# Kernel optimization log

Measured on AMD Instinct MI355X. Metric: run time of the kernel, lower is better.

## Reference

```python
import jax, jax.numpy as jnp
import numpy as np

B, N, C = 4, 1024, 1024
H, TD, MULT = 16, 256, 4
HD = C // H
MAX_LEN = 1024
EPS = 1e-5


def _layer_norm(x, g, b):
    m = jnp.mean(x, axis=-1, keepdims=True)
    v = jnp.mean((x - m) ** 2, axis=-1, keepdims=True)
    return (x - m) / jnp.sqrt(v + EPS) * g + b


def _skew(x):
    # x: [B,H,N,M] -> pad left on last dim, reshape, drop first row -> [B,H,N,M]
    b, h, n, m = x.shape
    x = jnp.pad(x, ((0, 0), (0, 0), (0, 0), (1, 0)))
    x = x.reshape(b, h, m + 1, n)
    return x[:, :, 1:, :]


def setup_inputs() -> dict:
    key = jax.random.key(0)
    ks = jax.random.split(key, 16)
    s = 0.02
    return {
        "x": jax.random.normal(ks[0], (B, N, C), jnp.float32),
        "t": jax.random.normal(ks[1], (B, TD), jnp.float32),
        "ln1_g": jnp.ones((C,), jnp.float32),
        "ln1_b": jnp.zeros((C,), jnp.float32),
        "qkv_w": jax.random.normal(ks[2], (C, 3 * C), jnp.float32) * s,
        "qkv_b": jnp.zeros((3 * C,), jnp.float32),
        "time_w": jax.random.normal(ks[3], (TD, 3 * C), jnp.float32) * s,
        "time_b": jnp.zeros((3 * C,), jnp.float32),
        "out_w": jax.random.normal(ks[4], (C, C), jnp.float32) * s,
        "out_b": jnp.zeros((C,), jnp.float32),
        "Er": jax.random.normal(ks[5], (MAX_LEN, HD), jnp.float32) * s,
        "ln2_g": jnp.ones((C,), jnp.float32),
        "ln2_b": jnp.zeros((C,), jnp.float32),
        "ff1_w": jax.random.normal(ks[6], (C, MULT * C), jnp.float32) * s,
        "ff1_b": jnp.zeros((MULT * C,), jnp.float32),
        "ff2_w": jax.random.normal(ks[7], (MULT * C, C), jnp.float32) * s,
        "ff2_b": jnp.zeros((C,), jnp.float32),
    }


def reference(x, t, ln1_g, ln1_b, qkv_w, qkv_b, time_w, time_b, out_w, out_b,
              Er, ln2_g, ln2_b, ff1_w, ff1_b, ff2_w, ff2_b):
    # ---- attention branch ----
    xn = _layer_norm(x, ln1_g, ln1_b)
    qkv = (xn @ qkv_w + qkv_b).reshape(B, N, 3, H, HD).transpose(2, 0, 3, 1, 4)
    q, k, v = qkv[0], qkv[1], qkv[2]  # [B,H,N,HD]
    tqkv = (t @ time_w + time_b).reshape(B, 1, 3, H, HD).transpose(2, 0, 3, 1, 4)
    q = q + tqkv[0]
    k = k + tqkv[1]
    v = v + tqkv[2]
    Er_n = Er[MAX_LEN - N:]  # [N,HD]
    rel = jnp.einsum('bhnd,md->bhnm', q, Er_n)
    rel = _skew(rel)
    scale = HD ** -0.5
    attn = jnp.einsum('bhnd,bhmd->bhnm', q, k) * scale + rel
    attn = jax.nn.softmax(attn, axis=-1)
    out = jnp.einsum('bhnm,bhmd->bhnd', attn, v)
    out = out.transpose(0, 2, 1, 3).reshape(B, N, C)
    x = x + (out @ out_w + out_b)
    # ---- FFN branch ----
    h = _layer_norm(x, ln2_g, ln2_b)
    h = jax.nn.gelu(h @ ff1_w + ff1_b, approximate=False)
    x = x + (h @ ff2_w + ff2_b)
    return x
```

## Files before the change

### kernel.cpp

```cpp
#include <hip/hip_runtime.h>
#include <hip/hip_bf16.h>

typedef __attribute__((ext_vector_type(8))) short short8;
typedef __attribute__((ext_vector_type(4))) float f32x4;
typedef __attribute__((ext_vector_type(16))) float f32x16;

#define DEV __device__ __forceinline__

DEV float bf2f(ushort u){ union { float f; unsigned int i; } x; x.i = ((unsigned int)u)<<16; return x.f; }
DEV ushort f2bf(float f){ union { float fl; unsigned int i; } x; x.fl = f; unsigned int r = x.i + 0x7fffu + ((x.i>>16)&1u); return (ushort)(r>>16); }

DEV void gl2lds16(const ushort* g, ushort* l){
  __builtin_amdgcn_global_load_lds((const __attribute__((address_space(1))) void*)g,
                                   (__attribute__((address_space(3))) void*)l, 16, 0, 0);
}
DEV f32x16 mfma32(short8 a, short8 b, f32x16 c){
  return __builtin_amdgcn_mfma_f32_32x32x16_bf16(a, b, c, 0, 0, 0);
}
DEV uint cvtpk(float lo, float hi){
  uint r; asm("v_cvt_pk_bf16_f32 %0, %1, %2" : "=v"(r) : "v"(lo), "v"(hi));
  return r;
}
DEV uint q8(float v){
  float c = fminf(fmaxf(v, -127.f), 127.f);
  return ((uint)(int)rintf(c)) & 255u;
}

__global__ void cvt_f2b(const float* __restrict__ in, ushort* __restrict__ out, int n){
  int i = blockIdx.x*blockDim.x + threadIdx.x;
  int stride = gridDim.x*blockDim.x;
  for (; i < n; i += stride) out[i] = f2bf(in[i]);
}

__global__ __launch_bounds__(256) void wt_cvt(const float* __restrict__ in, ushort* __restrict__ out,
                                              int K, int N, int ldk){
  const int n0 = blockIdx.x*64, k0 = blockIdx.y*64;
  __shared__ float T[64][65];
  const int tid = threadIdx.x;
  const int r = tid>>4, c = (tid&15)*4;
  #pragma unroll
  for (int p=0;p<4;p++){
    float4 v = *(const float4*)&in[(size_t)(k0 + p*16 + r)*N + n0 + c];
    T[p*16+r][c+0]=v.x; T[p*16+r][c+1]=v.y; T[p*16+r][c+2]=v.z; T[p*16+r][c+3]=v.w;
  }
  __syncthreads();
  #pragma unroll
  for (int p=0;p<4;p++){
    int n = p*16 + r;
    ushort u0 = f2bf(T[c+0][n]), u1 = f2bf(T[c+1][n]), u2 = f2bf(T[c+2][n]), u3 = f2bf(T[c+3][n]);
    ushort4 u = make_ushort4(u0,u1,u2,u3);
    *(ushort4*)&out[(size_t)(n0+n)*ldk + k0 + c] = u;
  }
}

__global__ __launch_bounds__(256) void vt_k(const ushort* __restrict__ qkv, ushort* __restrict__ vt){
  const int bh = blockIdx.y; const int b = bh>>4, h = bh&15;
  const int n0 = blockIdx.x*64;
  __shared__ ushort T[64][66];
  const int tid = threadIdx.x;
  const int r = tid>>3, c8 = (tid&7)*8;
  #pragma unroll
  for (int p=0;p<2;p++){
    int row = p*32 + r;
    short8 v = *(const short8*)&qkv[(size_t)(b*1024 + n0 + row)*3200 + 2048 + h*64 + c8];
    #pragma unroll
    for (int i=0;i<8;i++) T[row][c8+i] = ((ushort*)&v)[i];
  }
  __syncthreads();
  #pragma unroll
  for (int p=0;p<2;p++){
    int d = p*32 + r;
    union { ushort u[8]; short8 v; } o;
    #pragma unroll
    for (int i=0;i<8;i++) o.u[i] = T[c8+i][d];
    *(short8*)&vt[(size_t)(bh*64 + d)*1152 + n0 + c8] = o.v;
  }
}

__global__ __launch_bounds__(256) void ln_rows(const float* __restrict__ in,
                                               const float* __restrict__ g,
                                               const float* __restrict__ bta,
                                               ushort* __restrict__ out, int ldo){
  int row = blockIdx.x; int tid = threadIdx.x;
  const float* x = in + (size_t)row*1024;
  float v[4]; float s = 0.f;
  #pragma unroll
  for (int i=0;i<4;i++){ v[i] = x[tid + 256*i]; s += v[i]; }
  __shared__ float rbuf[256];
  rbuf[tid] = s; __syncthreads();
  for (int off=128; off>0; off>>=1){ if (tid<off) rbuf[tid]+=rbuf[tid+off]; __syncthreads(); }
  float mean = rbuf[0] * (1.f/1024.f);
  __syncthreads();
  float s2 = 0.f;
  #pragma unroll
  for (int i=0;i<4;i++){ float d=v[i]-mean; s2 += d*d; }
  rbuf[tid] = s2; __syncthreads();
  for (int off=128; off>0; off>>=1){ if (tid<off) rbuf[tid]+=rbuf[tid+off]; __syncthreads(); }
  float var = rbuf[0] * (1.f/1024.f);
  float rstd = rsqrtf(var + 1e-5f);
  #pragma unroll
  for (int i=0;i<4;i++){ int c = tid+256*i; out[(size_t)row*ldo+c] = f2bf((v[i]-mean)*rstd*g[c]+bta[c]); }
}

__global__ __launch_bounds__(256) void tq_gemm2(const float* __restrict__ t, const float* __restrict__ tw,
                                                const float* __restrict__ tb, float* __restrict__ tq){
  const int tid = threadIdx.x;
  const int j = blockIdx.x*64 + (tid & 63);
  const int sl = tid >> 6;
  float acc[4] = {0.f,0.f,0.f,0.f};
  for (int k = sl*64; k < sl*64+64; ++k){
    float wv = tw[(size_t)k*3072 + j];
    #pragma unroll
    for (int b=0;b<4;b++) acc[b] = fmaf(t[b*256+k], wv, acc[b]);
  }
  __shared__ float red[4][4][64];
  #pragma unroll
  for (int b=0;b<4;b++) red[sl][b][tid&63] = acc[b];
  __syncthreads();
  if (sl == 0){
    #pragma unroll
    for (int b=0;b<4;b++)
      tq[b*3072 + j] = red[0][b][tid&63] + red[1][b][tid&63] + red[2][b][tid&63] + red[3][b][tid&63] + tb[j];
  }
}

template<int EPI, int TN>
__global__ __launch_bounds__(256) void gemm4(
    const ushort* __restrict__ A, const ushort* __restrict__ Bt,
    const float* __restrict__ bias, const float* __restrict__ extra,
    ushort* __restrict__ outb, float* __restrict__ outf,
    int K, int lda, int ldb, int ldo, int lde, int nbx)
{
  constexpr int NJ = TN/32;
  __shared__ __align__(16) ushort Al[2][128*32];
  __shared__ __align__(16) ushort Bl[2][TN*32];
  const int nwg = gridDim.x, cpx = nwg >> 3;
  const int bid = blockIdx.x;
  const int swz = (bid & 7)*cpx + (bid >> 3);
  const int m0 = (swz / nbx)*128, n0 = (swz % nbx)*TN;
  const int tid = threadIdx.x, lane = tid & 63, wid = tid >> 6;
  const int wm = (wid&1)*64, wn = (wid>>1)*(TN/2);
  const int l15 = lane&15, l4 = lane>>4;
  f32x4 acc[4][NJ];
  #pragma unroll
  for (int i=0;i<4;i++)
    #pragma unroll
    for (int jx=0;jx<NJ;jx++){ acc[i][jx][0]=0.f; acc[i][jx][1]=0.f; acc[i][jx][2]=0.f; acc[i][jx][3]=0.f; }
  const ushort* a0p = A + (size_t)(m0 + (tid>>2))*lda + (tid&3)*8;
  const ushort* a1p = A + (size_t)(m0 + 64 + (tid>>2))*lda + (tid&3)*8;
  const ushort* b0p = Bt + (size_t)(n0 + (tid>>2))*ldb + (tid&3)*8;
  const ushort* b1p = nullptr;
  if constexpr (TN==128) b1p = Bt + (size_t)(n0 + 64 + (tid>>2))*ldb + (tid&3)*8;
  const int lsl = tid*8, lsh = (tid+256)*8;

  gl2lds16(a0p, &Al[0][lsl]);
  gl2lds16(a1p, &Al[0][lsh]);
  gl2lds16(b0p, &Bl[0][lsl]);
  if constexpr (TN==128) gl2lds16(b1p, &Bl[0][lsh]);
  __syncthreads();

  const int nk = K >> 5;
  for (int it=0; it<nk; ++it){
    const int cur = it & 1;
    ushort* Ac = Al[cur];  ushort* Bc = Bl[cur];
    if (it+1 < nk){
      const int k1 = (it+1) << 5;
      gl2lds16(a0p + k1, &Al[cur^1][lsl]);
      gl2lds16(a1p + k1, &Al[cur^1][lsh]);
      gl2lds16(b0p + k1, &Bl[cur^1][lsl]);
      if constexpr (TN==128) gl2lds16(b1p + k1, &Bl[cur^1][lsh]);
    }
    short8 af[4], bfr[NJ];
    #pragma unroll
    for (int mi=0;mi<4;mi++) af[mi]  = *(const short8*)&Ac[(wm + mi*16 + l15)*32 + l4*8];
    #pragma unroll
    for (int nj=0;nj<NJ;nj++) bfr[nj] = *(const short8*)&Bc[(wn + nj*16 + l15)*32 + l4*8];
    #pragma unroll
    for (int mi=0;mi<4;mi++)
      #pragma unroll
      for (int nj=0;nj<NJ;nj++)
        acc[mi][nj] = __builtin_amdgcn_mfma_f32_16x16x32_bf16(af[mi], bfr[nj], acc[mi][nj], 0,0,0);
    __syncthreads();
  }
  #pragma unroll
  for (int mi=0;mi<4;mi++)
    #pragma unroll
    for (int nj=0;nj<NJ;nj++)
      #pragma unroll
      for (int j=0;j<4;j++){
        int row = m0 + wm + mi*16 + l4*4 + j;
        int col = n0 + wn + nj*16 + l15;
        float v = acc[mi][nj][j] + bias[col];
        if constexpr (EPI==0){ v += extra[(size_t)(row>>10)*lde + col]; outb[(size_t)row*ldo+col] = f2bf(v); }
        else if constexpr (EPI==1){ v += extra[(size_t)row*lde + col]; outf[(size_t)row*ldo+col] = v; }
        else { v = 0.5f*v*(1.f+erff(v*0.70710678118f)); outb[(size_t)row*ldo+col] = f2bf(v); }
      }
}

__global__ __launch_bounds__(256) void attn8b(
    const ushort* __restrict__ qkv, const ushort* __restrict__ Er,
    const ushort* __restrict__ Vt, ushort* __restrict__ out)
{
  const int bid0 = blockIdx.x;
  const int swz = (bid0 & 7)*256 + (bid0 >> 3);
  const int bh = swz >> 5, b = bh >> 4, h = bh & 15;
  const int rt = swz & 31;
  const int r0 = rt*32;
  const int tid = threadIdx.x, w = tid >> 6, lane = tid & 63;
  const int l31 = lane & 31, hi = lane >> 5;

  __shared__ __align__(16) signed char RRF8[34704];
  ushort* Obuf = (ushort*)RRF8;
  float*  ml   = (float*)(RRF8 + 34192);

  const ushort* Qp = qkv + (size_t)b*1024*3200 + h*64;
  const ushort* Kp = Qp + 1024;
  const ushort* Vp = Vt + (size_t)bh*64*1152;

  const int r = r0 + l31;
  short8 qf0 = *(const short8*)(Qp + (size_t)r*3200 +      hi*8);
  short8 qf1 = *(const short8*)(Qp + (size_t)r*3200 + 16 + hi*8);
  short8 qf2 = *(const short8*)(Qp + (size_t)r*3200 + 32 + hi*8);
  short8 qf3 = *(const short8*)(Qp + (size_t)r*3200 + 48 + hi*8);

  if (tid < 32) RRF8[tid*1036 + 1035] = 0;

  const float ESC = 92.332481f;
  for (int t=0; t<8; ++t){
    const int e0 = w*256 + t*32;
    const ushort* ep = Er + (size_t)(e0 + l31)*64 + hi*8;
    short8 ea0 = *(const short8*)(ep);
    short8 ea1 = *(const short8*)(ep + 16);
    short8 ea2 = *(const short8*)(ep + 32);
    short8 ea3 = *(const short8*)(ep + 48);
    f32x16 acc = {};
    acc = mfma32(ea0, qf0, acc);
    acc = mfma32(ea1, qf1, acc);
    acc = mfma32(ea2, qf2, acc);
    acc = mfma32(ea3, qf3, acc);
    #pragma unroll
    for (int q=0;q<4;q++){
      int e = e0 + 8*q + 4*hi;
      uint u = q8(acc[4*q+0]*ESC) | (q8(acc[4*q+1]*ESC)<<8)
             | (q8(acc[4*q+2]*ESC)<<16) | (q8(acc[4*q+3]*ESC)<<24);
      *(uint*)(RRF8 + l31*1036 + e) = u;
    }
  }
  {
    const int q32r = min(r0 + 32, 1023);
    const ushort* q32 = Qp + (size_t)q32r*3200;
    const int e4 = tid*4;
    float a[4] = {0.f,0.f,0.f,0.f};
    #pragma unroll
    for (int c8=0;c8<8;c8++){
      short8 qv = *(const short8*)(q32 + c8*8);
      float qx[8];
      #pragma unroll
      for (int i=0;i<8;i++) qx[i] = bf2f(((ushort*)&qv)[i]);
      #pragma unroll
      for (int e=0;e<4;e++){
        short8 ev = *(const short8*)(Er + (size_t)(e4+e)*64 + c8*8);
        #pragma unroll
        for (int i=0;i<8;i++) a[e] = fmaf(qx[i], bf2f(((ushort*)&ev)[i]), a[e]);
      }
    }
    uint u = q8(a[0]*ESC) | (q8(a[1]*ESC)<<8) | (q8(a[2]*ESC)<<16) | (q8(a[3]*ESC)<<24);
    *(uint*)(RRF8 + 33152 + e4) = u;
  }
  __syncthreads();

  const int rbase = l31*1036;
  const int kvbase = w*256;
  f32x16 O0 = {}, O1 = {};
  float lsum = 0.f;

  short8 kA0 = *(const short8*)(Kp + (size_t)(kvbase + l31)*3200 +      hi*8);
  short8 kA1 = *(const short8*)(Kp + (size_t)(kvbase + l31)*3200 + 16 + hi*8);
  short8 kA2 = *(const short8*)(Kp + (size_t)(kvbase + l31)*3200 + 32 + hi*8);
  short8 kA3 = *(const short8*)(Kp + (size_t)(kvbase + l31)*3200 + 48 + hi*8);
  short8 kB0, kB1, kB2, kB3;

  auto step = [&](short8& ka0, short8& ka1, short8& ka2, short8& ka3,
                  short8& kn0, short8& kn1, short8& kn2, short8& kn3, int t){
    const int c0 = kvbase + t*32;
    if (t < 7){
      const ushort* kp = Kp + (size_t)(c0 + 32 + l31)*3200 + hi*8;
      kn0 = *(const short8*)(kp);
      kn1 = *(const short8*)(kp + 16);
      kn2 = *(const short8*)(kp + 32);
      kn3 = *(const short8*)(kp + 48);
    }
    signed char bs[16];
    #pragma unroll
    for (int q=0;q<4;q++)
      #pragma unroll
      for (int j=0;j<4;j++){
        int c = c0 + 8*q + 4*hi + j;
        int d = c - r;
        int off = (d<=0) ? (1023+d) : (1034+d);
        bs[4*q+j] = RRF8[rbase + off];
      }
    short8 v00 = *(const short8*)(Vp + (size_t)l31*1152      + c0 +      hi*8);
    short8 v01 = *(const short8*)(Vp + (size_t)l31*1152      + c0 + 16 + hi*8);
    short8 v10 = *(const short8*)(Vp + (size_t)(32+l31)*1152 + c0 +      hi*8);
    short8 v11 = *(const short8*)(Vp + (size_t)(32+l31)*1152 + c0 + 16 + hi*8);
    f32x16 S = {};
    __builtin_amdgcn_s_setprio(1);
    S = mfma32(ka0, qf0, S);
    S = mfma32(ka1, qf1, S);
    S = mfma32(ka2, qf2, S);
    S = mfma32(ka3, qf3, S);
    __builtin_amdgcn_s_setprio(0);
    float p[16];
    float s0=0.f, s1=0.f, s2=0.f, s3=0.f;
    #pragma unroll
    for (int i=0;i<16;i++){
      p[i] = __builtin_amdgcn_exp2f(fmaf(S[i], 0.18033688f, (float)bs[i]*0.015625f));
      if ((i&3)==0) s0 += p[i]; else if ((i&3)==1) s1 += p[i];
      else if ((i&3)==2) s2 += p[i]; else s3 += p[i];
    }
    lsum += (s0+s1)+(s2+s3);
    uint W00=cvtpk(p[0],p[1]),   W01=cvtpk(p[2],p[3]);
    uint W10=cvtpk(p[4],p[5]),   W11=cvtpk(p[6],p[7]);
    uint W20=cvtpk(p[8],p[9]),   W21=cvtpk(p[10],p[11]);
    uint W30=cvtpk(p[12],p[13]), W31=cvtpk(p[14],p[15]);
    uint x00 = (uint)__shfl_xor((int)(hi? W00 : W10), 32, 64);
    uint x01 = (uint)__shfl_xor((int)(hi? W01 : W11), 32, 64);
    uint x10 = (uint)__shfl_xor((int)(hi? W20 : W30), 32, 64);
    uint x11 = (uint)__shfl_xor((int)(hi? W21 : W31), 32, 64);
    union { uint u[4]; short8 v; } pf0, pf1;
    pf0.u[0] = hi ? x00 : W00;  pf0.u[1] = hi ? x01 : W01;
    pf0.u[2] = hi ? W10 : x00;  pf0.u[3] = hi ? W11 : x01;
    pf1.u[0] = hi ? x10 : W20;  pf1.u[1] = hi ? x11 : W21;
    pf1.u[2] = hi ? W30 : x10;  pf1.u[3] = hi ? W31 : x11;
    __builtin_amdgcn_s_setprio(1);
    O0 = mfma32(v00, pf0.v, O0);
    O0 = mfma32(v01, pf1.v, O0);
    O1 = mfma32(v10, pf0.v, O1);
    O1 = mfma32(v11, pf1.v, O1);
    __builtin_amdgcn_s_setprio(0);
  };
  for (int t=0;t<8;t+=2){
    step(kA0,kA1,kA2,kA3, kB0,kB1,kB2,kB3, t);
    step(kB0,kB1,kB2,kB3, kA0,kA1,kA2,kA3, t+1);
  }
  lsum = lsum + __shfl_xor(lsum, 32, 64);

  __syncthreads();
  #pragma unroll
  for (int q=0;q<4;q++){
    int d = 8*q + 4*hi;
    uint2 w0, w1;
    w0.x = cvtpk(O0[4*q+0], O0[4*q+1]); w0.y = cvtpk(O0[4*q+2], O0[4*q+3]);
    w1.x = cvtpk(O1[4*q+0], O1[4*q+1]); w1.y = cvtpk(O1[4*q+2], O1[4*q+3]);
    *(uint2*)&Obuf[(w*32 + l31)*68 + d] = w0;
    *(uint2*)&Obuf[(w*32 + l31)*68 + 32 + d] = w1;
  }
  if (hi == 0) ml[w*32 + l31] = lsum;
  __syncthreads();
  {
    const int row = tid >> 3, ds8 = (tid & 7)*8;
    float den = ml[row] + ml[32+row] + ml[64+row] + ml[96+row];
    float inv = 1.f/den;
    float num[8] = {0.f,0.f,0.f,0.f,0.f,0.f,0.f,0.f};
    #pragma unroll
    for (int w2=0;w2<4;w2++){
      uint2 o0 = *(const uint2*)&Obuf[(w2*32 + row)*68 + ds8];
      uint2 o1 = *(const uint2*)&Obuf[(w2*32 + row)*68 + ds8 + 4];
      const ushort* ou0 = (const ushort*)&o0;
      const ushort* ou1 = (const ushort*)&o1;
      #pragma unroll
      for (int i=0;i<4;i++){ num[i] += bf2f(ou0[i]); num[4+i] += bf2f(ou1[i]); }
    }
    union { uint u[4]; short8 v; } ov;
    ov.u[0] = cvtpk(num[0]*inv, num[1]*inv);
    ov.u[1] = cvtpk(num[2]*inv, num[3]*inv);
    ov.u[2] = cvtpk(num[4]*inv, num[5]*inv);
    ov.u[3] = cvtpk(num[6]*inv, num[7]*inv);
    *(short8*)&out[((size_t)(b*1024 + r0 + row))*1152 + h*64 + ds8] = ov.v;
  }
}

extern "C" void kernel_launch(void* const* d_in, const int* in_sizes, int n_in,
                              void* d_out, int out_size, void* d_ws, size_t ws_size,
                              hipStream_t stream)
{
  const float* x    = (const float*)d_in[0];
  const float* t    = (const float*)d_in[1];
  const float* ln1g = (const float*)d_in[2];
  const float* ln1b = (const float*)d_in[3];
  const float* qkvw = (const float*)d_in[4];
  const float* qkvb = (const float*)d_in[5];
  const float* timew= (const float*)d_in[6];
  const float* timeb= (const float*)d_in[7];
  const float* outw = (const float*)d_in[8];
  const float* outbv= (const float*)d_in[9];
  const float* Er   = (const float*)d_in[10];
  const float* ln2g = (const float*)d_in[11];
  const float* ln2b = (const float*)d_in[12];
  const float* ff1w = (const float*)d_in[13];
  const float* ff1b = (const float*)d_in[14];
  const float* ff2w = (const float*)d_in[15];
  const float* ff2b = (const float*)d_in[16];
  float* o = (float*)d_out;

  char* ws = (char*)d_ws;
  ushort* qkvw_t = (ushort*)(ws);
  ushort* outw_t = (ushort*)(ws + 7077888);
  ushort* ff1w_t = (ushort*)(ws + 9437184);
  ushort* ff2w_t = (ushort*)(ws + 18874368);
  ushort* er_b   = (ushort*)(ws + 27525120);
  float*  tq     = (float*) (ws + 27656192);
  ushort* bufA   = (ushort*)(ws + 27705344);
  ushort* vt     = (ushort*)(ws + 37142528);
  ushort* bufB   = (ushort*)(ws + 46579712);

  wt_cvt<<<dim3(48,16),256,0,stream>>>(qkvw, qkvw_t, 1024, 3072, 1152);
  wt_cvt<<<dim3(16,16),256,0,stream>>>(outw, outw_t, 1024, 1024, 1152);
  wt_cvt<<<dim3(64,16),256,0,stream>>>(ff1w, ff1w_t, 1024, 4096, 1152);
  wt_cvt<<<dim3(16,64),256,0,stream>>>(ff2w, ff2w_t, 4096, 1024, 4224);
  cvt_f2b<<<256,256,0,stream>>>(Er, er_b, 65536);

  ln_rows<<<4096,256,0,stream>>>(x, ln1g, ln1b, bufA, 1152);
  tq_gemm2<<<48,256,0,stream>>>(t, timew, timeb, tq);
  gemm4<0,128><<<768,256,0,stream>>>(bufA, qkvw_t, qkvb, tq, bufB, nullptr,
                                     1024, 1152, 1152, 3200, 3072, 24);
  vt_k<<<dim3(16,64),256,0,stream>>>(bufB, vt);
  attn8b<<<2048,256,0,stream>>>(bufB, er_b, vt, bufA);
  gemm4<1,64><<<512,256,0,stream>>>(bufA, outw_t, outbv, x, nullptr, o,
                                    1024, 1152, 1152, 1024, 1024, 16);
  ln_rows<<<4096,256,0,stream>>>(o, ln2g, ln2b, bufA, 1152);
  gemm4<2,128><<<1024,256,0,stream>>>(bufA, ff1w_t, ff1b, nullptr, bufB, nullptr,
                                      1024, 1152, 1152, 4224, 0, 32);
  gemm4<1,64><<<512,256,0,stream>>>(bufB, ff2w_t, ff2b, o, nullptr, o,
                                    4096, 4224, 4224, 1024, 1024, 16);
}
```

Baseline: 395.5 us.

## Split skewed relative-position bias into separate int8 precompute kernel

Adds a relskew8 kernel that computes Q·Er with MFMA, applies the skew in LDS, and writes an int8 bias matrix of shape B*H*1024*1040 to global workspace. The attention kernel then reads the bias directly from global memory instead of recomputing it per block. Each wave now owns 32 query rows across all 1024 keys, so the cross-wave reduction through LDS is gone and each wave normalizes and stores its own output. The cost is a large int8 bias round-trip through HBM (about 68MB written and read) plus an extra launch, and attention drops to 512 blocks with a long serial key loop.

```diff
diff --git a/kernel.cpp b/kernel.cpp
--- a/kernel.cpp
+++ b/kernel.cpp
@@ -197,109 +197,114 @@
       }
 }
 
-__global__ __launch_bounds__(256) void attn8b(
+__global__ __launch_bounds__(256) void relskew8(
     const ushort* __restrict__ qkv, const ushort* __restrict__ Er,
+    signed char* __restrict__ srel)
+{
+  const int bid0 = blockIdx.x;
+  const int bid = ((bid0 & 7) << 9) | (bid0 >> 3);
+  const int rt = bid & 63, h = (bid>>6)&15, b = bid>>10;
+  const int bh = b*16 + h;
+  const int r0 = rt*16;
+  const int tid = threadIdx.x, w = tid>>6, lane = tid&63;
+  const int l15 = lane&15, l4 = lane>>4;
+  __shared__ __align__(16) ushort T[17*1032];
+  signed char* srb = srel + (size_t)bh*1024*1040;
+
+  if (tid < 17){
+    int tgt = r0 - 1 + tid;
+    int c = tgt + 1;
+    if (tgt >= 0 && c <= 1023) T[tid*1032 + c] = 0;
+  }
+  const ushort* Qp = qkv + (size_t)b*1024*3200 + h*64;
+  short8 qa0 = *(const short8*)(Qp + (size_t)(r0+l15)*3200 + l4*8);
+  short8 qa1 = *(const short8*)(Qp + (size_t)(r0+l15)*3200 + 32 + l4*8);
+  for (int t=0;t<16;++t){
+    const int et = w*16 + t;
+    short8 e0 = *(const short8*)(Er + (size_t)(et*16+l15)*64 + l4*8);
+    short8 e1 = *(const short8*)(Er + (size_t)(et*16+l15)*64 + 32 + l4*8);
+    f32x4 a0 = {0.f,0.f,0.f,0.f};
+    a0 = __builtin_amdgcn_mfma_f32_16x16x32_bf16(qa0, e0, a0, 0,0,0);
+    a0 = __builtin_amdgcn_mfma_f32_16x16x32_bf16(qa1, e1, a0, 0,0,0);
+    const int e = et*16 + l15;
+    #pragma unroll
+    for (int j=0;j<4;j++){
+      int lr = 4*l4 + j;
+      int r = r0 + lr;
+      ushort v = f2bf(a0[j] * 1.4426950408f);
+      bool below = (e >= 1023 - r);
+      int ldsrow = below ? (lr + 1) : lr;
+      int c = below ? (e + r - 1023) : (e + r + 1);
+      T[ldsrow*1032 + c] = v;
+    }
+  }
+  __syncthreads();
+  const int c4 = tid*4;
+  for (int i=0;i<17;++i){
+    int tgt = r0 - 1 + i;
+    if (tgt < 0) continue;
+    int lo = (i==0) ? (r0+1) : 0;
+    int hh = (i==16) ? min(r0+16,1023) : 1023;
+    if (c4 >= lo && c4+3 <= hh){
+      uint u = q8(bf2f(T[i*1032+c4+0])*64.f)
+             | (q8(bf2f(T[i*1032+c4+1])*64.f)<<8)
+             | (q8(bf2f(T[i*1032+c4+2])*64.f)<<16)
+             | (q8(bf2f(T[i*1032+c4+3])*64.f)<<24);
+      *(uint*)(srb + (size_t)tgt*1040 + c4) = u;
+    } else if (c4 <= hh && c4+3 >= lo){
+      #pragma unroll
+      for (int k2=0;k2<4;k2++){
+        int c = c4 + k2;
+        if (c >= lo && c <= hh)
+          srb[(size_t)tgt*1040 + c] = (signed char)(int)q8(bf2f(T[i*1032 + c])*64.f);
+      }
+    }
+  }
+}
+
+__global__ __launch_bounds__(256) void attn9(
+    const ushort* __restrict__ qkv, const signed char* __restrict__ srel,
     const ushort* __restrict__ Vt, ushort* __restrict__ out)
 {
   const int bid0 = blockIdx.x;
-  const int swz = (bid0 & 7)*256 + (bid0 >> 3);
-  const int bh = swz >> 5, b = bh >> 4, h = bh & 15;
-  const int rt = swz & 31;
-  const int r0 = rt*32;
+  const int swz = (bid0 & 7)*64 + (bid0 >> 3);
+  const int bh = swz >> 3, b = bh >> 4, h = bh & 15;
+  const int rblk = (swz & 7)*128;
   const int tid = threadIdx.x, w = tid >> 6, lane = tid & 63;
   const int l31 = lane & 31, hi = lane >> 5;
-
-  __shared__ __align__(16) signed char RRF8[34704];
-  ushort* Obuf = (ushort*)RRF8;
-  float*  ml   = (float*)(RRF8 + 34192);
-
+  const int r = rblk + w*32 + l31;
   const ushort* Qp = qkv + (size_t)b*1024*3200 + h*64;
   const ushort* Kp = Qp + 1024;
   const ushort* Vp = Vt + (size_t)bh*64*1152;
-
-  const int r = r0 + l31;
+  const signed char* Bp = srel + (size_t)bh*1024*1040 + (size_t)r*1040 + hi*4;
+
   short8 qf0 = *(const short8*)(Qp + (size_t)r*3200 +      hi*8);
   short8 qf1 = *(const short8*)(Qp + (size_t)r*3200 + 16 + hi*8);
   short8 qf2 = *(const short8*)(Qp + (size_t)r*3200 + 32 + hi*8);
   short8 qf3 = *(const short8*)(Qp + (size_t)r*3200 + 48 + hi*8);
 
-  if (tid < 32) RRF8[tid*1036 + 1035] = 0;
-
-  const float ESC = 92.332481f;
-  for (int t=0; t<8; ++t){
-    const int e0 = w*256 + t*32;
-    const ushort* ep = Er + (size_t)(e0 + l31)*64 + hi*8;
-    short8 ea0 = *(const short8*)(ep);
-    short8 ea1 = *(const short8*)(ep + 16);
-    short8 ea2 = *(const short8*)(ep + 32);
-    short8 ea3 = *(const short8*)(ep + 48);
-    f32x16 acc = {};
-    acc = mfma32(ea0, qf0, acc);
-    acc = mfma32(ea1, qf1, acc);
-    acc = mfma32(ea2, qf2, acc);
-    acc = mfma32(ea3, qf3, acc);
-    #pragma unroll
-    for (int q=0;q<4;q++){
-      int e = e0 + 8*q + 4*hi;
-      uint u = q8(acc[4*q+0]*ESC) | (q8(acc[4*q+1]*ESC)<<8)
-             | (q8(acc[4*q+2]*ESC)<<16) | (q8(acc[4*q+3]*ESC)<<24);
-      *(uint*)(RRF8 + l31*1036 + e) = u;
-    }
-  }
-  {
-    const int q32r = min(r0 + 32, 1023);
-    const ushort* q32 = Qp + (size_t)q32r*3200;
-    const int e4 = tid*4;
-    float a[4] = {0.f,0.f,0.f,0.f};
-    #pragma unroll
-    for (int c8=0;c8<8;c8++){
-      short8 qv = *(const short8*)(q32 + c8*8);
-      float qx[8];
-      #pragma unroll
-      for (int i=0;i<8;i++) qx[i] = bf2f(((ushort*)&qv)[i]);
-      #pragma unroll
-      for (int e=0;e<4;e++){
-        short8 ev = *(const short8*)(Er + (size_t)(e4+e)*64 + c8*8);
-        #pragma unroll
-        for (int i=0;i<8;i++) a[e] = fmaf(qx[i], bf2f(((ushort*)&ev)[i]), a[e]);
-      }
-    }
-    uint u = q8(a[0]*ESC) | (q8(a[1]*ESC)<<8) | (q8(a[2]*ESC)<<16) | (q8(a[3]*ESC)<<24);
-    *(uint*)(RRF8 + 33152 + e4) = u;
-  }
-  __syncthreads();
-
-  const int rbase = l31*1036;
-  const int kvbase = w*256;
   f32x16 O0 = {}, O1 = {};
   float lsum = 0.f;
 
-  short8 kA0 = *(const short8*)(Kp + (size_t)(kvbase + l31)*3200 +      hi*8);
-  short8 kA1 = *(const short8*)(Kp + (size_t)(kvbase + l31)*3200 + 16 + hi*8);
-  short8 kA2 = *(const short8*)(Kp + (size_t)(kvbase + l31)*3200 + 32 + hi*8);
-  short8 kA3 = *(const short8*)(Kp + (size_t)(kvbase + l31)*3200 + 48 + hi*8);
+  short8 kA0 = *(const short8*)(Kp + (size_t)l31*3200 +      hi*8);
+  short8 kA1 = *(const short8*)(Kp + (size_t)l31*3200 + 16 + hi*8);
+  short8 kA2 = *(const short8*)(Kp + (size_t)l31*3200 + 32 + hi*8);
+  short8 kA3 = *(const short8*)(Kp + (size_t)l31*3200 + 48 + hi*8);
   short8 kB0, kB1, kB2, kB3;
 
   auto step = [&](short8& ka0, short8& ka1, short8& ka2, short8& ka3,
                   short8& kn0, short8& kn1, short8& kn2, short8& kn3, int t){
-    const int c0 = kvbase + t*32;
-    if (t < 7){
+    const int c0 = t*32;
+    if (t < 31){
       const ushort* kp = Kp + (size_t)(c0 + 32 + l31)*3200 + hi*8;
       kn0 = *(const short8*)(kp);
       kn1 = *(const short8*)(kp + 16);
       kn2 = *(const short8*)(kp + 32);
       kn3 = *(const short8*)(kp + 48);
     }
-    signed char bs[16];
-    #pragma unroll
-    for (int q=0;q<4;q++)
-      #pragma unroll
-      for (int j=0;j<4;j++){
-        int c = c0 + 8*q + 4*hi + j;
-        int d = c - r;
-        int off = (d<=0) ? (1023+d) : (1034+d);
-        bs[4*q+j] = RRF8[rbase + off];
-      }
+    uint bw[4];
+    #pragma unroll
+    for (int rq=0;rq<4;rq++) bw[rq] = *(const uint*)(Bp + c0 + rq*8);
     short8 v00 = *(const short8*)(Vp + (size_t)l31*1152      + c0 +      hi*8);
     short8 v01 = *(const short8*)(Vp + (size_t)l31*1152      + c0 + 16 + hi*8);
     short8 v10 = *(const short8*)(Vp + (size_t)(32+l31)*1152 + c0 +      hi*8);
@@ -314,11 +319,14 @@
     float p[16];
     float s0=0.f, s1=0.f, s2=0.f, s3=0.f;
     #pragma unroll
-    for (int i=0;i<16;i++){
-      p[i] = __builtin_amdgcn_exp2f(fmaf(S[i], 0.18033688f, (float)bs[i]*0.015625f));
-      if ((i&3)==0) s0 += p[i]; else if ((i&3)==1) s1 += p[i];
-      else if ((i&3)==2) s2 += p[i]; else s3 += p[i];
-    }
+    for (int rq=0;rq<4;rq++)
+      #pragma unroll
+      for (int j=0;j<4;j++){
+        float bias = (float)(signed char)((bw[rq] >> (8*j)) & 255u) * 0.015625f;
+        float pv = __builtin_amdgcn_exp2f(fmaf(S[rq*4+j], 0.18033688f, bias));
+        p[rq*4+j] = pv;
+        if (j==0) s0 += pv; else if (j==1) s1 += pv; else if (j==2) s2 += pv; else s3 += pv;
+      }
     lsum += (s0+s1)+(s2+s3);
     uint W00=cvtpk(p[0],p[1]),   W01=cvtpk(p[2],p[3]);
     uint W10=cvtpk(p[4],p[5]),   W11=cvtpk(p[6],p[7]);
@@ -340,45 +348,23 @@
     O1 = mfma32(v11, pf1.v, O1);
     __builtin_amdgcn_s_setprio(0);
   };
-  for (int t=0;t<8;t+=2){
+  for (int t=0;t<32;t+=2){
     step(kA0,kA1,kA2,kA3, kB0,kB1,kB2,kB3, t);
     step(kB0,kB1,kB2,kB3, kA0,kA1,kA2,kA3, t+1);
   }
-  lsum = lsum + __shfl_xor(lsum, 32, 64);
-
-  __syncthreads();
-  #pragma unroll
-  for (int q=0;q<4;q++){
-    int d = 8*q + 4*hi;
-    uint2 w0, w1;
-    w0.x = cvtpk(O0[4*q+0], O0[4*q+1]); w0.y = cvtpk(O0[4*q+2], O0[4*q+3]);
-    w1.x = cvtpk(O1[4*q+0], O1[4*q+1]); w1.y = cvtpk(O1[4*q+2], O1[4*q+3]);
-    *(uint2*)&Obuf[(w*32 + l31)*68 + d] = w0;
-    *(uint2*)&Obuf[(w*32 + l31)*68 + 32 + d] = w1;
-  }
-  if (hi == 0) ml[w*32 + l31] = lsum;
-  __syncthreads();
-  {
-    const int row = tid >> 3, ds8 = (tid & 7)*8;
-    float den = ml[row] + ml[32+row] + ml[64+row] + ml[96+row];
-    float inv = 1.f/den;
-    float num[8] = {0.f,0.f,0.f,0.f,0.f,0.f,0.f,0.f};
-    #pragma unroll
-    for (int w2=0;w2<4;w2++){
-      uint2 o0 = *(const uint2*)&Obuf[(w2*32 + row)*68 + ds8];
-      uint2 o1 = *(const uint2*)&Obuf[(w2*32 + row)*68 + ds8 + 4];
-      const ushort* ou0 = (const ushort*)&o0;
-      const ushort* ou1 = (const ushort*)&o1;
-      #pragma unroll
-      for (int i=0;i<4;i++){ num[i] += bf2f(ou0[i]); num[4+i] += bf2f(ou1[i]); }
+  float inv = 1.f/(lsum + __shfl_xor(lsum, 32, 64));
+  ushort* op = out + ((size_t)(b*1024 + r))*1152 + h*64;
+  #pragma unroll
+  for (int rq=0;rq<4;rq++)
+    #pragma unroll
+    for (int s=0;s<2;s++){
+      int reg = rq*4 + s*2;
+      uint w0 = cvtpk(O0[reg]*inv, O0[reg+1]*inv);
+      uint w1 = cvtpk(O1[reg]*inv, O1[reg+1]*inv);
+      int d = rq*8 + hi*4 + s*2;
+      *(uint*)(op + d) = w0;
+      *(uint*)(op + 32 + d) = w1;
     }
-    union { uint u[4]; short8 v; } ov;
-    ov.u[0] = cvtpk(num[0]*inv, num[1]*inv);
-    ov.u[1] = cvtpk(num[2]*inv, num[3]*inv);
-    ov.u[2] = cvtpk(num[4]*inv, num[5]*inv);
-    ov.u[3] = cvtpk(num[6]*inv, num[7]*inv);
-    *(short8*)&out[((size_t)(b*1024 + r0 + row))*1152 + h*64 + ds8] = ov.v;
-  }
 }
 
 extern "C" void kernel_launch(void* const* d_in, const int* in_sizes, int n_in,
@@ -414,6 +400,7 @@
   ushort* bufA   = (ushort*)(ws + 27705344);
   ushort* vt     = (ushort*)(ws + 37142528);
   ushort* bufB   = (ushort*)(ws + 46579712);
+  signed char* srel8 = (signed char*)(ws + 81182720);
 
   wt_cvt<<<dim3(48,16),256,0,stream>>>(qkvw, qkvw_t, 1024, 3072, 1152);
   wt_cvt<<<dim3(16,16),256,0,stream>>>(outw, outw_t, 1024, 1024, 1152);
@@ -426,7 +413,8 @@
   gemm4<0,128><<<768,256,0,stream>>>(bufA, qkvw_t, qkvb, tq, bufB, nullptr,
                                      1024, 1152, 1152, 3200, 3072, 24);
   vt_k<<<dim3(16,64),256,0,stream>>>(bufB, vt);
-  attn8b<<<2048,256,0,stream>>>(bufB, er_b, vt, bufA);
+  relskew8<<<4096,256,0,stream>>>(bufB, er_b, srel8);
+  attn9<<<512,256,0,stream>>>(bufB, srel8, vt, bufA);
   gemm4<1,64><<<512,256,0,stream>>>(bufA, outw_t, outbv, x, nullptr, o,
                                     1024, 1152, 1152, 1024, 1024, 16);
   ln_rows<<<4096,256,0,stream>>>(o, ln2g, ln2b, bufA, 1152);
```

Measured after the change: 399.3 us. No clear change (+1.0%).
